# Kernel optimization log

Hardware: AMD Instinct MI355X
Metric: run time of the kernel (lower is better)

Reference implementation:

```python
import jax, jax.numpy as jnp
from jax import lax
import numpy as np

SCALE, K_UP = 2, 5


def conv2d(x, w, pad=0, dil=1):
    return lax.conv_general_dilated(x, w, (1, 1), [(pad, pad), (pad, pad)],
                                    rhs_dilation=(dil, dil),
                                    dimension_numbers=('NCHW', 'OIHW', 'NCHW'))


def cbr(x, w, g, b, pad=0, relu=True):
    # Conv (no bias) + BatchNorm (eval: running_mean=0, running_var=1, eps=1e-5) + optional ReLU
    x = conv2d(x, w, pad)
    x = x * (g / jnp.sqrt(1.0 + 1e-5))[None, :, None, None] + b[None, :, None, None]
    return jnp.maximum(x, 0.0) if relu else x


def resize_bilinear_ac(x, ho, wo):
    # bilinear interpolation, align_corners=True (matches F.interpolate)
    B, C, H, W = x.shape
    ys = jnp.linspace(0.0, H - 1.0, ho)
    xs = jnp.linspace(0.0, W - 1.0, wo)
    y0 = jnp.floor(ys).astype(jnp.int32); y1 = jnp.minimum(y0 + 1, H - 1)
    x0 = jnp.floor(xs).astype(jnp.int32); x1 = jnp.minimum(x0 + 1, W - 1)
    wy = (ys - y0).astype(x.dtype)
    wx = (xs - x0).astype(x.dtype)
    top = x[:, :, y0, :]
    bot = x[:, :, y1, :]
    v = top * (1.0 - wy)[None, None, :, None] + bot * wy[None, None, :, None]
    return v[:, :, :, x0] * (1.0 - wx) + v[:, :, :, x1] * wx


def setup_inputs() -> dict:
    key = jax.random.key(0)
    ks = jax.random.split(key, 10)
    B, CH, CL, H, W = 4, 256, 128, 64, 64
    CMID, CO, IC, KENC = 64, 128, 64, 3

    def wgt(k, shape):
        fan = int(np.prod(shape[1:]))
        return (jax.random.normal(k, shape, jnp.float32) / np.sqrt(fan)).astype(jnp.float32)

    d = {}
    d['x_h'] = jax.random.normal(ks[0], (B, CH, H, W), jnp.float32)
    d['x_l'] = jax.random.normal(ks[1], (B, CL, H * SCALE, W * SCALE), jnp.float32)
    d['w_reduce'] = wgt(ks[2], (IC, CH, 3, 3)); d['g_reduce'] = jnp.ones(IC); d['b_reduce'] = jnp.zeros(IC)
    d['w1'] = wgt(ks[3], (CMID, CH, 1, 1)); d['g1'] = jnp.ones(CMID); d['b1'] = jnp.zeros(CMID)
    d['w2'] = wgt(ks[4], (CMID, CL, 1, 1)); d['g2'] = jnp.ones(CMID); d['b2'] = jnp.zeros(CMID)
    d['w_enc'] = wgt(ks[5], (K_UP * K_UP, 2 * CMID, KENC, KENC)); d['g_enc'] = jnp.ones(K_UP * K_UP); d['b_enc'] = jnp.zeros(K_UP * K_UP)
    d['w_out1'] = wgt(ks[6], (CO, IC + CL, 3, 3)); d['g_out1'] = jnp.ones(CO); d['b_out1'] = jnp.zeros(CO)
    d['w_out2'] = wgt(ks[7], (CO, CO, 1, 1)); d['g_out2'] = jnp.ones(CO); d['b_out2'] = jnp.zeros(CO)
    return d


def reference(x_h, x_l, w_reduce, g_reduce, b_reduce, w1, g1, b1, w2, g2, b2,
              w_enc, g_enc, b_enc, w_out1, g_out1, b_out1, w_out2, g_out2, b_out2):
    b, c, h, w = x_h.shape
    h_, w_ = h * SCALE, w * SCALE
    # content encoder -> per-pixel reassembly kernels
    x1 = resize_bilinear_ac(cbr(x_h, w1, g1, b1), h_, w_)          # [b, cmid, h_, w_]
    x2 = cbr(x_l, w2, g2, b2)                                       # [b, cmid, h_, w_]
    Wm = cbr(jnp.concatenate([x1, x2], axis=1), w_enc, g_enc, b_enc, pad=1, relu=False)
    Wm = jax.nn.softmax(Wm, axis=1)                                  # [b, k_up^2, h_, w_]
    # reduced high-level features, upsampled
    xr = cbr(x_h, w_reduce, g_reduce, b_reduce, pad=1)               # [b, ic, h, w]
    xu = resize_bilinear_ac(xr, h_, w_)                              # [b, ic, h_, w_]
    # CARAFE-style reassembly: unfold(k=5, dilation=2, pad=4) expressed as
    # 25 shifted windows of the zero-padded map -> no k^2-blown buffer.
    pad = (K_UP // 2) * SCALE
    xp = jnp.pad(xu, ((0, 0), (0, 0), (pad, pad), (pad, pad)))
    X = jnp.zeros_like(xu)
    for i in range(K_UP):
        for j in range(K_UP):
            win = xp[:, :, i * SCALE:i * SCALE + h_, j * SCALE:j * SCALE + w_]
            X = X + Wm[:, i * K_UP + j][:, None] * win
    y = jnp.concatenate([X, x_l], axis=1)
    y = cbr(y, w_out1, g_out1, b_out1, pad=1)
    y = cbr(y, w_out2, g_out2, b_out2)
    return y
```

## Files before the change

kernel.cpp:

```cpp
#include <hip/hip_runtime.h>
#include <math.h>

#define BNS 0.99999500003749981f

typedef short          bf16x8  __attribute__((ext_vector_type(8)));
typedef float          f32x4   __attribute__((ext_vector_type(4)));
typedef unsigned short u16x8   __attribute__((ext_vector_type(8)));
typedef unsigned short u16x4   __attribute__((ext_vector_type(4)));
typedef unsigned short ushort_t;

__device__ inline ushort_t f2b(float f) {
    union { float f; unsigned int u; } x; x.f = f;
    unsigned int u = x.u;
    unsigned int r = (u + 0x7FFFu + ((u >> 16) & 1u)) >> 16;
    return (ushort_t)r;
}
__device__ inline float b2f(ushort_t s) {
    union { unsigned int u; float f; } x; x.u = ((unsigned int)s) << 16;
    return x.f;
}

__device__ inline void glds16(const ushort_t* gp, void* lp) {
    __builtin_amdgcn_global_load_lds(
        (const __attribute__((address_space(1))) unsigned int*)gp,
        (__attribute__((address_space(3))) unsigned int*)lp, 16, 0, 0);
}

template<int N, bool LG0>
__device__ __forceinline__ void wait_v() {
    if constexpr (LG0) {
        if constexpr (N == 0)  asm volatile("s_waitcnt vmcnt(0) lgkmcnt(0)" ::: "memory");
        if constexpr (N == 2)  asm volatile("s_waitcnt vmcnt(2) lgkmcnt(0)" ::: "memory");
        if constexpr (N == 3)  asm volatile("s_waitcnt vmcnt(3) lgkmcnt(0)" ::: "memory");
        if constexpr (N == 4)  asm volatile("s_waitcnt vmcnt(4) lgkmcnt(0)" ::: "memory");
        if constexpr (N == 5)  asm volatile("s_waitcnt vmcnt(5) lgkmcnt(0)" ::: "memory");
        if constexpr (N == 6)  asm volatile("s_waitcnt vmcnt(6) lgkmcnt(0)" ::: "memory");
        if constexpr (N == 8)  asm volatile("s_waitcnt vmcnt(8) lgkmcnt(0)" ::: "memory");
        if constexpr (N == 9)  asm volatile("s_waitcnt vmcnt(9) lgkmcnt(0)" ::: "memory");
        if constexpr (N == 10) asm volatile("s_waitcnt vmcnt(10) lgkmcnt(0)" ::: "memory");
        if constexpr (N == 12) asm volatile("s_waitcnt vmcnt(12) lgkmcnt(0)" ::: "memory");
        if constexpr (N == 16) asm volatile("s_waitcnt vmcnt(16) lgkmcnt(0)" ::: "memory");
    } else {
        if constexpr (N == 0)  asm volatile("s_waitcnt vmcnt(0)" ::: "memory");
        if constexpr (N == 2)  asm volatile("s_waitcnt vmcnt(2)" ::: "memory");
        if constexpr (N == 3)  asm volatile("s_waitcnt vmcnt(3)" ::: "memory");
        if constexpr (N == 4)  asm volatile("s_waitcnt vmcnt(4)" ::: "memory");
        if constexpr (N == 5)  asm volatile("s_waitcnt vmcnt(5)" ::: "memory");
        if constexpr (N == 6)  asm volatile("s_waitcnt vmcnt(6)" ::: "memory");
        if constexpr (N == 8)  asm volatile("s_waitcnt vmcnt(8)" ::: "memory");
        if constexpr (N == 9)  asm volatile("s_waitcnt vmcnt(9)" ::: "memory");
        if constexpr (N == 10) asm volatile("s_waitcnt vmcnt(10)" ::: "memory");
        if constexpr (N == 12) asm volatile("s_waitcnt vmcnt(12)" ::: "memory");
        if constexpr (N == 16) asm volatile("s_waitcnt vmcnt(16)" ::: "memory");
    }
}
#define WAITSW(nn, LG) do { switch (nn) {                       \
    case 0:  wait_v<0,  LG>(); break;                           \
    case 2:  wait_v<2,  LG>(); break;                           \
    case 3:  wait_v<3,  LG>(); break;                           \
    case 4:  wait_v<4,  LG>(); break;                           \
    case 5:  wait_v<5,  LG>(); break;                           \
    case 6:  wait_v<6,  LG>(); break;                           \
    case 8:  wait_v<8,  LG>(); break;                           \
    case 9:  wait_v<9,  LG>(); break;                           \
    case 10: wait_v<10, LG>(); break;                           \
    case 12: wait_v<12, LG>(); break;                           \
    default: wait_v<16, LG>(); break; } } while (0)

#define E_BWR   0u
#define E_BW1   147456u
#define E_BW2   163840u
#define E_BWE   172032u
#define E_BWO1  208896u
#define E_BWO2  430080u
#define E_ZP    446464u
#define OFF_R1  524288u
#define OFF_R4  4718592u
#define OFF_R2  8912896u
#define OFF_R3  9961472u
#define OFF_R6  11010048u
#define OFF_R5  13107200u


__device__ inline void wseg3(int idx, const float* src, ushort_t* dst,
                             int TAPS, int COT, int CIT, int CO_real) {
    int kt  = idx / (COT * 32);
    int r   = idx - kt * (COT * 32);
    int q   = r / (COT * 8);
    int r2  = r - q * (COT * 8);
    int co  = r2 >> 3;
    int e   = r2 & 7;
    int KCT = CIT >> 5;
    int tap = kt / KCT, j = kt - tap * KCT;
    int ci  = j * 32 + q * 8 + e;
    float v = (co < CO_real) ? src[((size_t)co * CIT + ci) * TAPS + tap] : 0.f;
    dst[idx] = f2b(v);
}

__device__ inline void cvt_t16(const float* __restrict__ in,
                               ushort_t* __restrict__ out,
                               int C, int LHW, int px, int npx) {
    if (px >= npx) return;
    int HW = 1 << LHW;
    int b = px >> LHW, phw = px & (HW - 1);
    const float* src = in + (size_t)b * C * HW + phw;
    unsigned base = (unsigned)(px >> 4) * (C * 16) + (unsigned)(px & 15) * 8;
    for (int c0 = 0; c0 < C; c0 += 8) {
        u16x8 o;
#pragma unroll
        for (int j = 0; j < 8; j++) o[j] = f2b(src[(size_t)(c0 + j) * HW]);
        *reinterpret_cast<u16x8*>(out + base + (c0 >> 3) * 128) = o;
    }
}

__global__ __launch_bounds__(256)
void prep_all(const float* wr, const float* w1, const float* w2,
              const float* we, const float* wo1, const float* wo2,
              const float* xh, const float* xl, ushort_t* ws0)
{
    int bx = blockIdx.x;
    int tid = threadIdx.x;
    if (bx < 1872) {
        int idx = bx * 256 + tid;
        const int n0 = 9*64*256;
        const int n1 = 64*256;
        const int n2 = 64*128;
        const int n3 = 9*32*128;
        const int n4 = 9*128*192;
        const int n5 = 128*128;
        if (idx < n0) { wseg3(idx, wr,  ws0 + E_BWR,  9, 64, 256, 64);  return; } idx -= n0;
        if (idx < n1) { wseg3(idx, w1,  ws0 + E_BW1,  1, 64, 256, 64);  return; } idx -= n1;
        if (idx < n2) { wseg3(idx, w2,  ws0 + E_BW2,  1, 64, 128, 64);  return; } idx -= n2;
        if (idx < n3) { wseg3(idx, we,  ws0 + E_BWE,  9, 32, 128, 25);  return; } idx -= n3;
        if (idx < n4) { wseg3(idx, wo1, ws0 + E_BWO1, 9, 128, 192, 128); return; } idx -= n4;
        if (idx < n5) { wseg3(idx, wo2, ws0 + E_BWO2, 1, 128, 128, 128); return; } idx -= n5;
        if (idx < 32768) ws0[E_ZP + idx] = 0;
        return;
    }
    bx -= 1872;
    if (bx < 64) { cvt_t16(xh, ws0 + OFF_R1, 256, 12, bx * 256 + tid, 16384); return; }
    bx -= 64;
    cvt_t16(xl, ws0 + OFF_R5, 128, 14, bx * 256 + tid, 65536);
}

__global__ __launch_bounds__(256)
void conv_dual(const ushort_t* __restrict__ ws0,
               unsigned offA, unsigned offWr, unsigned offW1,
               const float* __restrict__ gR, const float* __restrict__ bR,
               const float* __restrict__ g1, const float* __restrict__ b1,
               ushort_t* __restrict__ outR, ushort_t* __restrict__ outC)
{
    constexpr int BM = 64, BN = 64, KCT = 8, DEP = 3, NPH = 24;
    constexpr int MF = 2, NF = 2;
    constexpr int WOFF = BM * 64;
    constexpr int ZS   = WOFF + 4 * BN * 64;
    constexpr int BUF  = ZS + 16;
    __shared__ __align__(16) char lds[DEP * BUF];

    const unsigned nx = gridDim.x, ox = blockIdx.x;
    const unsigned qq = nx >> 3, xcd = ox & 7, k0 = ox >> 3;
    const unsigned bx = xcd * qq + k0;

    const int tid = threadIdx.x, w = tid >> 6, lane = tid & 63;
    const int l15 = lane & 15, lhi = lane >> 4;
    const int wpx = (w & 1) * 32, cw0 = (w >> 1) * 32;
    const int yb = (int)(bx & 63u);
    const unsigned pxc0 = bx * 4;

    if (tid < 4 * DEP) *(unsigned*)(lds + (tid >> 2) * BUF + ZS + (tid & 3) * 4) = 0u;

    int aA[3][MF];
#pragma unroll
    for (int dxi = 0; dxi < 3; ++dxi)
#pragma unroll
        for (int mf = 0; mf < MF; ++mf) {
            int pr = wpx + mf * 16 + l15 + dxi - 1;
            bool ok = (pr >= 0) && (pr < BM);
            aA[dxi][mf] = ok ? (((pr >> 4) << 10) + (lhi << 8) + ((pr & 15) << 4)) : ZS;
        }
    int wA[NF];
#pragma unroll
    for (int nf = 0; nf < NF; ++nf)
        wA[nf] = lhi * 1024 + (cw0 + nf * 16 + l15) * 16;

    f32x4 acc[NF][MF], acc2[NF][MF];
#pragma unroll
    for (int nf = 0; nf < NF; ++nf)
#pragma unroll
        for (int mf = 0; mf < MF; ++mf) {
            acc[nf][mf]  = (f32x4){0.f, 0.f, 0.f, 0.f};
            acc2[nf][mf] = (f32x4){0.f, 0.f, 0.f, 0.f};
        }

    auto stage = [&](int p, int bsel) {
        char* lb = lds + bsel * BUF;
        const int dyi = p >> 3, kc = p & 7;
        const int dy = dyi - 1;
        const bool rowv = (yb + dy >= 0) && (yb + dy < 64);
        unsigned s = rowv
            ? offA + (unsigned)((int)pxc0 + dy * 4 + w) * 4096u
                   + (unsigned)(kc * 512) + (unsigned)(lane * 8)
            : E_ZP + (unsigned)(lane * 8);
        glds16(ws0 + s, lb + w * 1024);
#pragma unroll
        for (int i = 0; i < 3; ++i) {
            int t3 = i * 4 + w;
            int tl = t3 >> 2, uu = t3 & 3;
            unsigned wsrc = offWr + (unsigned)(((dyi * 3 + tl) * KCT + kc) * 2048)
                          + (unsigned)(uu * 512) + (unsigned)(lane * 8);
            glds16(ws0 + wsrc, lb + WOFF + tl * 4096 + uu * 1024);
        }
        if (dyi == 1) {
            unsigned wsrc = offW1 + (unsigned)(kc * 2048)
                          + (unsigned)(w * 512) + (unsigned)(lane * 8);
            glds16(ws0 + wsrc, lb + WOFF + 3 * 4096 + w * 1024);
        }
    };

    auto step = [&](int p, int bsel) {
        const char* lb = lds + bsel * BUF;
        const int dyi = p >> 3;
        __builtin_amdgcn_s_setprio(1);
#pragma unroll
        for (int t = 0; t < 3; ++t) {
            bf16x8 af[MF], wf[NF];
#pragma unroll
            for (int mf = 0; mf < MF; ++mf)
                af[mf] = *reinterpret_cast<const bf16x8*>(lb + aA[t][mf]);
#pragma unroll
            for (int nf = 0; nf < NF; ++nf)
                wf[nf] = *reinterpret_cast<const bf16x8*>(lb + WOFF + t * 4096 + wA[nf]);
#pragma unroll
            for (int nf = 0; nf < NF; ++nf)
#pragma unroll
                for (int mf = 0; mf < MF; ++mf)
                    acc[nf][mf] = __builtin_amdgcn_mfma_f32_16x16x32_bf16(
                        wf[nf], af[mf], acc[nf][mf], 0, 0, 0);
        }
        if (dyi == 1) {
            bf16x8 af[MF], wf[NF];
#pragma unroll
            for (int mf = 0; mf < MF; ++mf)
                af[mf] = *reinterpret_cast<const bf16x8*>(lb + aA[1][mf]);
#pragma unroll
            for (int nf = 0; nf < NF; ++nf)
                wf[nf] = *reinterpret_cast<const bf16x8*>(lb + WOFF + 3 * 4096 + wA[nf]);
#pragma unroll
            for (int nf = 0; nf < NF; ++nf)
#pragma unroll
                for (int mf = 0; mf < MF; ++mf)
                    acc2[nf][mf] = __builtin_amdgcn_mfma_f32_16x16x32_bf16(
                        wf[nf], af[mf], acc2[nf][mf], 0, 0, 0);
        }
        __builtin_amdgcn_s_setprio(0);
    };

    stage(0, 0); stage(1, 1);
#pragma unroll
    for (int p = 0; p < NPH; ++p) {
        if (p + 2 < NPH) stage(p + 2, (p + 2) % 3);
        int n1 = (p + 1 < NPH) ? ((((p + 1) >> 3) == 1) ? 5 : 4) : 0;
        int n2 = (p + 2 < NPH) ? ((((p + 2) >> 3) == 1) ? 5 : 4) : 0;
        int nn = n1 + n2;
        if (p == 0) WAITSW(nn, true); else WAITSW(nn, false);
        __builtin_amdgcn_s_barrier();
        __builtin_amdgcn_sched_barrier(0);
        step(p, p % 3);
        __builtin_amdgcn_sched_barrier(0);
        if (p + 1 < NPH) __builtin_amdgcn_s_barrier();
    }

#pragma unroll
    for (int which = 0; which < 2; ++which) {
        const float* gg = which ? g1 : gR;
        const float* bb = which ? b1 : bR;
        ushort_t* oo = which ? outC : outR;
#pragma unroll
        for (int nf = 0; nf < NF; ++nf) {
            const int cg = cw0 + nf * 16 + (lhi << 2);
            float sc[4], bi[4];
#pragma unroll
            for (int r = 0; r < 4; r++) { sc[r] = gg[cg + r] * BNS; bi[r] = bb[cg + r]; }
#pragma unroll
            for (int mf = 0; mf < MF; ++mf) {
                f32x4 a = which ? acc2[nf][mf] : acc[nf][mf];
                u16x4 ov;
#pragma unroll
                for (int r = 0; r < 4; r++)
                    ov[r] = f2b(fmaxf(fmaf(a[r], sc[r], bi[r]), 0.f));
                int px = (int)bx * BM + wpx + mf * 16 + l15;
                unsigned off = (unsigned)(px >> 4) * 1024
                             + (unsigned)(cg >> 3) * 128
                             + (unsigned)(px & 15) * 8 + (unsigned)(cg & 7);
                *reinterpret_cast<u16x4*>(oo + off) = ov;
            }
        }
    }
}

template<int TAPS, int BM, int CIA, int CIB, int COT, int BN, int G,
         int WSX, int DEP, int EPI>
__global__ __launch_bounds__(256)
void conv_lds(const ushort_t* __restrict__ ws0,
              unsigned offA, unsigned offB, unsigned offW,
              const float* __restrict__ g, const float* __restrict__ bia,
              int COclamp, void* __restrict__ outp,
              int H, int LHW, int relu)
{
    constexpr int KCA = CIA / 32, KCB = CIB / 32;
    constexpr int KCT = KCA + KCB;
    constexpr int NW  = (TAPS == 9) ? 3 : G;
    constexpr int ACP = (TAPS == 9) ? 1 : G;
    constexpr int NPH = (TAPS == 9) ? 3 * KCT : KCT / G;
    constexpr int WSY = 4 / WSX;
    constexpr int MF = BM / WSX / 16;
    constexpr int NF = BN / WSY / 16;
    constexpr int ACHUNK = BM / 16;
    constexpr int A4 = (ACP * ACHUNK + 3) / 4;
    constexpr int WUNIT = BN / 16;
    constexpr int TWU = NW * WUNIT;
    constexpr int W4 = (TWU + 3) / 4;
    constexpr int SS = A4 + W4;
    constexpr int WOFF = ACP * BM * 64;
    constexpr int ZS   = WOFF + NW * BN * 64;
    constexpr int BUF  = ZS + 16;
    constexpr int LBN3 = (BN == 128) ? 10 : (BN == 64) ? 9 : 8;
    __shared__ __align__(16) char lds[DEP * BUF];

    const unsigned nx = gridDim.x, ox = blockIdx.x;
    const unsigned qq = nx >> 3, xcd = ox & 7, k0 = ox >> 3;
    const unsigned bx = xcd * qq + k0;
    const int co_blk = blockIdx.y * BN;

    const int tid = threadIdx.x, w = tid >> 6, lane = tid & 63;
    const int l15 = lane & 15, lhi = lane >> 4;
    const int wpx = (w % WSX) * (BM / WSX);
    const int cw0 = (w / WSX) * (BN / WSY);
    const int yb = (int)(bx & (unsigned)(H - 1));
    const unsigned pxc0 = bx * ACHUNK;

    if (tid < 4 * DEP) *(unsigned*)(lds + (tid >> 2) * BUF + ZS + (tid & 3) * 4) = 0u;

    int aA[3][MF];
#pragma unroll
    for (int dxi = 0; dxi < 3; ++dxi) {
        const int dx = dxi - 1;
#pragma unroll
        for (int mf = 0; mf < MF; ++mf) {
            int pr = wpx + mf * 16 + l15 + dx;
            bool ok = (TAPS == 1) ? true : (pr >= 0 && pr < BM);
            aA[dxi][mf] = ok ? (((pr >> 4) << 10) + (lhi << 8) + ((pr & 15) << 4)) : ZS;
        }
    }
    int wA[NF];
#pragma unroll
    for (int nf = 0; nf < NF; ++nf)
        wA[nf] = (lhi * BN + cw0 + nf * 16 + l15) * 16;

    f32x4 acc[NF][MF];
#pragma unroll
    for (int nf = 0; nf < NF; ++nf)
#pragma unroll
        for (int mf = 0; mf < MF; ++mf)
            acc[nf][mf] = (f32x4){0.f, 0.f, 0.f, 0.f};

    auto stage = [&](int p, int bsel) {
        char* lb = lds + bsel * BUF;
        if constexpr (TAPS == 9) {
            const int dyi = p / KCT, kc = p - dyi * KCT;
            const int dy = dyi - 1;
            const bool isA = (kc < KCA);
            const int kcs = isA ? kc : kc - KCA;
            const int CI  = isA ? CIA : CIB;
            const unsigned offS = isA ? offA : offB;
            const bool rowv = (yb + dy >= 0) && (yb + dy < H);
#pragma unroll
            for (int i = 0; i < A4; ++i) {
                int u = (i * 4 + w) % ACHUNK;
                unsigned s = rowv
                    ? offS + (unsigned)((int)pxc0 + dy * ACHUNK + u) * (unsigned)(CI * 16)
                           + (unsigned)(kcs * 512) + (unsigned)(lane * 8)
                    : E_ZP + (unsigned)(lane * 8);
                glds16(ws0 + s, lb + u * 1024);
            }
#pragma unroll
            for (int i = 0; i < W4; ++i) {
                int t3 = (i * 4 + w) % TWU;
                int tl = t3 / WUNIT, uu = t3 - tl * WUNIT;
                unsigned wsrc = offW + (unsigned)((dyi * 3 + tl) * KCT + kc)
                                       * (unsigned)(COT * 32);
                int el  = uu * 512 + lane * 8;
                int q   = el >> LBN3;
                int col = (el & ((1 << LBN3) - 1)) >> 3;
                glds16(ws0 + wsrc + q * (COT * 8) + (co_blk + col) * 8,
                       lb + WOFF + tl * (BN * 64) + uu * 1024);
            }
        } else {
#pragma unroll
            for (int i = 0; i < A4; ++i) {
                int lin = (i * 4 + w) % (ACP * ACHUNK);
                int gc = lin / ACHUNK, u = lin - gc * ACHUNK;
                unsigned s = offA + (unsigned)(pxc0 + u) * (unsigned)(CIA * 16)
                           + (unsigned)((p * G + gc) * 512) + (unsigned)(lane * 8);
                glds16(ws0 + s, lb + gc * (BM * 64) + u * 1024);
            }
#pragma unroll
            for (int i = 0; i < W4; ++i) {
                int t3 = (i * 4 + w) % TWU;
                int tl = t3 / WUNIT, uu = t3 - tl * WUNIT;
                unsigned wsrc = offW + (unsigned)(p * G + tl) * (unsigned)(COT * 32);
                int el  = uu * 512 + lane * 8;
                int q   = el >> LBN3;
                int col = (el & ((1 << LBN3) - 1)) >> 3;
                glds16(ws0 + wsrc + q * (COT * 8) + (co_blk + col) * 8,
                       lb + WOFF + tl * (BN * 64) + uu * 1024);
            }
        }
    };

    auto step = [&](int p, int bsel) {
        const char* lb = lds + bsel * BUF;
        __builtin_amdgcn_s_setprio(1);
#pragma unroll
        for (int t = 0; t < NW; ++t) {
            const int dxi = (TAPS == 9) ? t : 1;
            const char* ab = lb + ((TAPS == 9) ? 0 : t * (BM * 64));
            bf16x8 af[MF], wf[NF];
#pragma unroll
            for (int mf = 0; mf < MF; ++mf)
                af[mf] = *reinterpret_cast<const bf16x8*>(ab + aA[dxi][mf]);
#pragma unroll
            for (int nf = 0; nf < NF; ++nf)
                wf[nf] = *reinterpret_cast<const bf16x8*>(
                    lb + WOFF + t * (BN * 64) + wA[nf]);
#pragma unroll
            for (int nf = 0; nf < NF; ++nf)
#pragma unroll
                for (int mf = 0; mf < MF; ++mf)
                    acc[nf][mf] = __builtin_amdgcn_mfma_f32_16x16x32_bf16(
                        wf[nf], af[mf], acc[nf][mf], 0, 0, 0);
        }
        __builtin_amdgcn_s_setprio(0);
    };

    stage(0, 0);
    if constexpr (DEP == 3) { if (1 < NPH) stage(1, 1); }
#pragma unroll
    for (int p = 0; p < NPH; ++p) {
        if (p + DEP - 1 < NPH) stage(p + DEP - 1, (p + DEP - 1) % DEP);
        int rem = NPH - 1 - p;
        int nn = (rem >= DEP - 1 ? DEP - 1 : rem) * SS;
        if (p == 0) WAITSW(nn, true); else WAITSW(nn, false);
        __builtin_amdgcn_s_barrier();
        __builtin_amdgcn_sched_barrier(0);
        step(p, p % DEP);
        __builtin_amdgcn_sched_barrier(0);
        if (p + 1 < NPH) __builtin_amdgcn_s_barrier();
    }

    if constexpr (EPI == 0) {
        ushort_t* o1 = (ushort_t*)outp;
#pragma unroll
        for (int nf = 0; nf < NF; ++nf) {
            const int cg = co_blk + cw0 + nf * 16 + (lhi << 2);
            float sc[4], bi[4];
#pragma unroll
            for (int r = 0; r < 4; r++) {
                int c = min(cg + r, COclamp - 1);
                sc[r] = g[c] * BNS; bi[r] = bia[c];
            }
#pragma unroll
            for (int mf = 0; mf < MF; ++mf) {
                f32x4 a = acc[nf][mf];
                u16x4 ov;
#pragma unroll
                for (int r = 0; r < 4; r++) {
                    float v = fmaf(a[r], sc[r], bi[r]);
                    if (relu) v = fmaxf(v, 0.f);
                    ov[r] = f2b(v);
                }
                int px = (int)bx * BM + wpx + mf * 16 + l15;
                unsigned off = (unsigned)(px >> 4) * (COT * 16)
                             + (unsigned)(cg >> 3) * 128
                             + (unsigned)(px & 15) * 8 + (unsigned)(cg & 7);
                *reinterpret_cast<u16x4*>(o1 + off) = ov;
            }
        }
    } else if constexpr (EPI == 1) {
        float* o1 = (float*)outp;
        const int HW = 1 << LHW;
#pragma unroll
        for (int nf = 0; nf < NF; ++nf) {
            const int cg = co_blk + cw0 + nf * 16 + (lhi << 2);
            float sc[4], bi[4];
#pragma unroll
            for (int r = 0; r < 4; r++) {
                int c = min(cg + r, COclamp - 1);
                sc[r] = g[c] * BNS; bi[r] = bia[c];
            }
#pragma unroll
            for (int mf = 0; mf < MF; ++mf) {
                int px = (int)bx * BM + wpx + mf * 16 + l15;
                int b = px >> LHW, phw = px & (HW - 1);
#pragma unroll
                for (int r = 0; r < 4; r++) {
                    float v = fmaf(acc[nf][mf][r], sc[r], bi[r]);
                    if (relu) v = fmaxf(v, 0.f);
                    o1[((size_t)(b * COT + cg + r)) * HW + phw] = v;
                }
            }
        }
    } else if constexpr (EPI == 2) {
        __syncthreads();
        float* sf = (float*)lds;
#pragma unroll
        for (int nf = 0; nf < NF; ++nf) {
            const int cg = cw0 + nf * 16 + (lhi << 2);
#pragma unroll
            for (int mf = 0; mf < MF; ++mf) {
                int pxl = wpx + mf * 16 + l15;
                f32x4 a = acc[nf][mf];
#pragma unroll
                for (int r = 0; r < 4; r++) {
                    int c = min(cg + r, COclamp - 1);
                    sf[(cg + r) * 136 + pxl] = fmaf(a[r], g[c] * BNS, bia[c]);
                }
            }
        }
        __syncthreads();
        if (tid < BM) {
            int gpx = (int)bx * BM + tid;
            float v[25];
#pragma unroll
            for (int c = 0; c < 25; ++c) v[c] = sf[c * 136 + tid];
            float m = v[0];
#pragma unroll
            for (int c = 1; c < 25; ++c) m = fmaxf(m, v[c]);
            float s = 0.f;
#pragma unroll
            for (int c = 0; c < 25; ++c) { v[c] = __expf(v[c] - m); s += v[c]; }
            float inv = 1.f / s;
            ushort_t* o1 = (ushort_t*)outp;
            unsigned base = (unsigned)(gpx >> 4) * (32 * 16) + (unsigned)(gpx & 15) * 8;
#pragma unroll
            for (int q = 0; q < 3; ++q) {
                u16x8 ov;
#pragma unroll
                for (int k = 0; k < 8; k++) ov[k] = f2b(v[q * 8 + k] * inv);
                *reinterpret_cast<u16x8*>(o1 + base + q * 128) = ov;
            }
            o1[base + 384] = f2b(v[24] * inv);
        }
    } else {
        float* o1 = (float*)outp;
        float* sf = (float*)lds;
        const int phw_base = (int)((bx & 127u) * 128);
        const int bimg = (int)(bx >> 7);
        const int lane32 = tid & 31, cog = tid >> 5;
#pragma unroll
        for (int c = 0; c < 2; ++c) {
            __syncthreads();
            if (cw0 == c * 64) {
#pragma unroll
                for (int nf = 0; nf < NF; ++nf) {
                    const int cgl = nf * 16 + (lhi << 2);
                    const int cg  = c * 64 + cgl;
                    float sc[4], bi[4];
#pragma unroll
                    for (int r = 0; r < 4; r++) { sc[r] = g[cg + r] * BNS; bi[r] = bia[cg + r]; }
#pragma unroll
                    for (int mf = 0; mf < MF; ++mf) {
                        int pxl = wpx + mf * 16 + l15;
                        f32x4 a = acc[nf][mf];
#pragma unroll
                        for (int r = 0; r < 4; r++) {
                            float v = fmaf(a[r], sc[r], bi[r]);
                            if (relu) v = fmaxf(v, 0.f);
                            sf[(cgl + r) * 132 + pxl] = v;
                        }
                    }
                }
            }
            __syncthreads();
#pragma unroll
            for (int j = 0; j < 8; ++j) {
                int col = cog + j * 8;
                f32x4 v = *reinterpret_cast<const f32x4*>(sf + col * 132 + lane32 * 4);
                *reinterpret_cast<f32x4*>(
                    o1 + (((size_t)bimg * 128 + c * 64 + col) << 14)
                       + phw_base + lane32 * 4) = v;
            }
        }
    }
}

__global__ __launch_bounds__(256)
void resize2x_t16(const ushort_t* __restrict__ in, ushort_t* __restrict__ out)
{
    int t = blockIdx.x * 256 + threadIdx.x;
    int cg = t & 7;
    int opx = t >> 3;
    int xo = opx & 127;
    int rest = opx >> 7;
    int yo = rest & 127;
    int b  = rest >> 7;
    float fy = (float)yo * 63.f / 127.f;
    float fx = (float)xo * 63.f / 127.f;
    int y0 = (int)fy, x0 = (int)fx;
    float wy = fy - (float)y0, wx = fx - (float)x0;
    int y1 = min(y0 + 1, 63), x1 = min(x0 + 1, 63);
    int qb = b * 4096;
#define RD(Y, X) (*reinterpret_cast<const bf16x8*>(in + \
    (unsigned)(((qb + (Y) * 64 + (X)) >> 4) * 1024) + cg * 128 + ((qb + (Y) * 64 + (X)) & 15) * 8))
    bf16x8 v00 = RD(y0, x0), v01 = RD(y0, x1), v10 = RD(y1, x0), v11 = RD(y1, x1);
#undef RD
    u16x8 o;
#pragma unroll
    for (int k = 0; k < 8; k++) {
        float l = b2f((ushort_t)v00[k]) * (1.f - wy) + b2f((ushort_t)v10[k]) * wy;
        float r = b2f((ushort_t)v01[k]) * (1.f - wy) + b2f((ushort_t)v11[k]) * wy;
        o[k] = f2b(l * (1.f - wx) + r * wx);
    }
    *reinterpret_cast<u16x8*>(out + (unsigned)(opx >> 4) * 1024 + cg * 128 + (opx & 15) * 8) = o;
}

__global__ __launch_bounds__(256)
void carafe25(const ushort_t* __restrict__ wm, const ushort_t* __restrict__ xu,
              ushort_t* __restrict__ out)
{
    int t = blockIdx.x * 256 + threadIdx.x;
    int cg = t & 7;
    int px = t >> 3;
    int x = px & 127;
    int y = (px >> 7) & 127;
    const ushort_t* wp = wm + (unsigned)(px >> 4) * 512 + (px & 15) * 8;
    u16x8 r0 = *reinterpret_cast<const u16x8*>(wp);
    u16x8 r1 = *reinterpret_cast<const u16x8*>(wp + 128);
    u16x8 r2 = *reinterpret_cast<const u16x8*>(wp + 256);
    float v[25];
#pragma unroll
    for (int k = 0; k < 8; k++) v[k]      = b2f(r0[k]);
#pragma unroll
    for (int k = 0; k < 8; k++) v[8 + k]  = b2f(r1[k]);
#pragma unroll
    for (int k = 0; k < 8; k++) v[16 + k] = b2f(r2[k]);
    v[24] = b2f(wp[384]);

    float acc[8];
#pragma unroll
    for (int k = 0; k < 8; k++) acc[k] = 0.f;
#pragma unroll
    for (int i = 0; i < 5; i++) {
        int yy = y + 2 * i - 4;
#pragma unroll
        for (int j = 0; j < 5; j++) {
            int xx = x + 2 * j - 4;
            if (yy >= 0 && yy < 128 && xx >= 0 && xx < 128) {
                int q = px + (2 * i - 4) * 128 + (2 * j - 4);
                bf16x8 xv = *reinterpret_cast<const bf16x8*>(
                    xu + (unsigned)(q >> 4) * 1024 + cg * 128 + (q & 15) * 8);
                float wv = v[i * 5 + j];
#pragma unroll
                for (int k = 0; k < 8; k++)
                    acc[k] = fmaf(wv, b2f((ushort_t)xv[k]), acc[k]);
            }
        }
    }
    u16x8 o;
#pragma unroll
    for (int k = 0; k < 8; k++) o[k] = f2b(acc[k]);
    *reinterpret_cast<u16x8*>(out + (unsigned)(px >> 4) * 1024 + cg * 128 + (px & 15) * 8) = o;
}

extern "C" void kernel_launch(void* const* d_in, const int* in_sizes, int n_in,
                              void* d_out, int out_size, void* d_ws, size_t ws_size,
                              hipStream_t stream)
{
    const float* x_h      = (const float*)d_in[0];
    const float* x_l      = (const float*)d_in[1];
    const float* w_reduce = (const float*)d_in[2];
    const float* g_reduce = (const float*)d_in[3];
    const float* b_reduce = (const float*)d_in[4];
    const float* w1       = (const float*)d_in[5];
    const float* g1       = (const float*)d_in[6];
    const float* b1       = (const float*)d_in[7];
    const float* w2       = (const float*)d_in[8];
    const float* g2       = (const float*)d_in[9];
    const float* b2       = (const float*)d_in[10];
    const float* w_enc    = (const float*)d_in[11];
    const float* g_enc    = (const float*)d_in[12];
    const float* b_enc    = (const float*)d_in[13];
    const float* w_out1   = (const float*)d_in[14];
    const float* g_out1   = (const float*)d_in[15];
    const float* b_out1   = (const float*)d_in[16];
    const float* w_out2   = (const float*)d_in[17];
    const float* g_out2   = (const float*)d_in[18];
    const float* b_out2   = (const float*)d_in[19];

    ushort_t* ws0 = (ushort_t*)d_ws;

    const unsigned oXHC = OFF_R1;
    const unsigned oC1  = OFF_R2;
    const unsigned oXR  = OFF_R3;
    const unsigned oX1  = OFF_R4;
    const unsigned oXLC = OFF_R5;
    const unsigned oX2  = OFF_R1;
    const unsigned oWM  = OFF_R6;
    const unsigned oXU  = OFF_R4;
    const unsigned oXB  = OFF_R1;
    const unsigned oY1  = OFF_R4;

    prep_all<<<2192, 256, 0, stream>>>(w_reduce, w1, w2, w_enc, w_out1, w_out2,
                                       x_h, x_l, ws0);
    conv_dual<<<256, 256, 0, stream>>>(
        ws0, oXHC, E_BWR, E_BW1, g_reduce, b_reduce, g1, b1,
        ws0 + oXR, ws0 + oC1);
    resize2x_t16<<<2048, 256, 0, stream>>>(ws0 + oC1, ws0 + oX1);
    conv_lds<1, 128, 128, 0, 64, 64, 1, 2, 3, 0><<<dim3(512, 1), 256, 0, stream>>>(
        ws0, oXLC, 0u, E_BW2, g2, b2, 64, ws0 + oX2, 128, 14, 1);
    conv_lds<9, 128, 64, 64, 32, 32, 1, 4, 3, 2><<<dim3(512, 1), 256, 0, stream>>>(
        ws0, oX1, oX2, E_BWE, g_enc, b_enc, 25, ws0 + oWM, 128, 14, 0);
    resize2x_t16<<<2048, 256, 0, stream>>>(ws0 + oXR, ws0 + oXU);
    carafe25<<<2048, 256, 0, stream>>>(ws0 + oWM, ws0 + oXU, ws0 + oXB);
    conv_lds<9, 128, 64, 128, 128, 128, 1, 2, 2, 0><<<dim3(512, 1), 256, 0, stream>>>(
        ws0, oXB, oXLC, E_BWO1, g_out1, b_out1, 128, ws0 + oY1, 128, 14, 1);
    conv_lds<1, 128, 128, 0, 128, 128, 2, 2, 2, 3><<<dim3(512, 1), 256, 0, stream>>>(
        ws0, oY1, 0u, E_BWO2, g_out2, b_out2, 128, d_out, 128, 14, 1);
}
```

Baseline: 133.9 us.

## Fuse final 1x1 conv into the 3x3 output conv epilogue

The last 3x3 conv+BN+ReLU now keeps its 128-pixel by 128-channel bf16 result tile in LDS. The same block loads the 1x1 weights and runs a second MFMA GEMM over it, then writes the fp32 output directly. This drops one kernel launch and the global round-trip of the intermediate Y1 tensor. In exchange the block does more work serially in its epilogue and uses more LDS and registers (a second accumulator array), which may lower occupancy.

```diff
diff --git a/kernel.cpp b/kernel.cpp
--- a/kernel.cpp
+++ b/kernel.cpp
@@ -305,7 +305,9 @@
               unsigned offA, unsigned offB, unsigned offW,
               const float* __restrict__ g, const float* __restrict__ bia,
               int COclamp, void* __restrict__ outp,
-              int H, int LHW, int relu)
+              int H, int LHW, int relu,
+              unsigned offW2, const float* __restrict__ g2,
+              const float* __restrict__ bia2)
 {
     constexpr int KCA = CIA / 32, KCB = CIB / 32;
     constexpr int KCT = KCA + KCB;
@@ -552,6 +554,67 @@
             o1[base + 384] = f2b(v[24] * inv);
         }
     } else {
+#pragma unroll
+        for (int nf = 0; nf < NF; ++nf) {
+            const int cg = cw0 + nf * 16 + (lhi << 2);
+            float sc[4], bi[4];
+#pragma unroll
+            for (int r = 0; r < 4; r++) { sc[r] = g[cg + r] * BNS; bi[r] = bia[cg + r]; }
+#pragma unroll
+            for (int mf = 0; mf < MF; ++mf) {
+                f32x4 a = acc[nf][mf];
+                u16x4 ov;
+#pragma unroll
+                for (int r = 0; r < 4; r++)
+                    ov[r] = f2b(fmaxf(fmaf(a[r], sc[r], bi[r]), 0.f));
+                int pxl = wpx + mf * 16 + l15;
+                unsigned off = (unsigned)(pxl >> 4) * 4096
+                             + (unsigned)(cg >> 5) * 1024
+                             + (unsigned)((cg >> 3) & 3) * 256
+                             + (unsigned)(pxl & 15) * 16 + (unsigned)(cg & 7) * 2;
+                *reinterpret_cast<u16x4*>((char*)lds + off) = ov;
+            }
+        }
+        __syncthreads();
+#pragma unroll
+        for (int i = 0; i < 8; ++i) {
+            int U = i * 4 + w;
+            glds16(ws0 + offW2 + (unsigned)U * 512 + (unsigned)(lane * 8),
+                   lds + BUF + U * 1024);
+        }
+        wait_v<0, true>();
+        __builtin_amdgcn_s_barrier();
+        __builtin_amdgcn_sched_barrier(0);
+        f32x4 acc2[NF][MF];
+#pragma unroll
+        for (int nf = 0; nf < NF; ++nf)
+#pragma unroll
+            for (int mf = 0; mf < MF; ++mf)
+                acc2[nf][mf] = (f32x4){0.f, 0.f, 0.f, 0.f};
+        __builtin_amdgcn_s_setprio(1);
+#pragma unroll
+        for (int kc = 0; kc < 4; ++kc) {
+            bf16x8 af[MF], wf[NF];
+#pragma unroll
+            for (int mf = 0; mf < MF; ++mf) {
+                int pxl = wpx + mf * 16 + l15;
+                af[mf] = *reinterpret_cast<const bf16x8*>(
+                    (char*)lds + (pxl >> 4) * 4096 + kc * 1024
+                               + (lhi << 8) + (pxl & 15) * 16);
+            }
+#pragma unroll
+            for (int nf = 0; nf < NF; ++nf)
+                wf[nf] = *reinterpret_cast<const bf16x8*>(
+                    (char*)lds + BUF + kc * 8192 + wA[nf]);
+#pragma unroll
+            for (int nf = 0; nf < NF; ++nf)
+#pragma unroll
+                for (int mf = 0; mf < MF; ++mf)
+                    acc2[nf][mf] = __builtin_amdgcn_mfma_f32_16x16x32_bf16(
+                        wf[nf], af[mf], acc2[nf][mf], 0, 0, 0);
+        }
+        __builtin_amdgcn_s_setprio(0);
+        __syncthreads();
         float* o1 = (float*)outp;
         float* sf = (float*)lds;
         const int phw_base = (int)((bx & 127u) * 128);
@@ -559,7 +622,7 @@
         const int lane32 = tid & 31, cog = tid >> 5;
 #pragma unroll
         for (int c = 0; c < 2; ++c) {
-            __syncthreads();
+            if (c) __syncthreads();
             if (cw0 == c * 64) {
 #pragma unroll
                 for (int nf = 0; nf < NF; ++nf) {
@@ -567,17 +630,15 @@
                     const int cg  = c * 64 + cgl;
                     float sc[4], bi[4];
 #pragma unroll
-                    for (int r = 0; r < 4; r++) { sc[r] = g[cg + r] * BNS; bi[r] = bia[cg + r]; }
+                    for (int r = 0; r < 4; r++) { sc[r] = g2[cg + r] * BNS; bi[r] = bia2[cg + r]; }
 #pragma unroll
                     for (int mf = 0; mf < MF; ++mf) {
                         int pxl = wpx + mf * 16 + l15;
-                        f32x4 a = acc[nf][mf];
-#pragma unroll
-                        for (int r = 0; r < 4; r++) {
-                            float v = fmaf(a[r], sc[r], bi[r]);
-                            if (relu) v = fmaxf(v, 0.f);
-                            sf[(cgl + r) * 132 + pxl] = v;
-                        }
+                        f32x4 a = acc2[nf][mf];
+#pragma unroll
+                        for (int r = 0; r < 4; r++)
+                            sf[(cgl + r) * 132 + pxl] =
+                                fmaxf(fmaf(a[r], sc[r], bi[r]), 0.f);
                     }
                 }
             }
@@ -708,7 +769,6 @@
     const unsigned oWM  = OFF_R6;
     const unsigned oXU  = OFF_R4;
     const unsigned oXB  = OFF_R1;
-    const unsigned oY1  = OFF_R4;
 
     prep_all<<<2192, 256, 0, stream>>>(w_reduce, w1, w2, w_enc, w_out1, w_out2,
                                        x_h, x_l, ws0);
@@ -717,13 +777,14 @@
         ws0 + oXR, ws0 + oC1);
     resize2x_t16<<<2048, 256, 0, stream>>>(ws0 + oC1, ws0 + oX1);
     conv_lds<1, 128, 128, 0, 64, 64, 1, 2, 3, 0><<<dim3(512, 1), 256, 0, stream>>>(
-        ws0, oXLC, 0u, E_BW2, g2, b2, 64, ws0 + oX2, 128, 14, 1);
+        ws0, oXLC, 0u, E_BW2, g2, b2, 64, ws0 + oX2, 128, 14, 1,
+        0u, nullptr, nullptr);
     conv_lds<9, 128, 64, 64, 32, 32, 1, 4, 3, 2><<<dim3(512, 1), 256, 0, stream>>>(
-        ws0, oX1, oX2, E_BWE, g_enc, b_enc, 25, ws0 + oWM, 128, 14, 0);
+        ws0, oX1, oX2, E_BWE, g_enc, b_enc, 25, ws0 + oWM, 128, 14, 0,
+        0u, nullptr, nullptr);
     resize2x_t16<<<2048, 256, 0, stream>>>(ws0 + oXR, ws0 + oXU);
     carafe25<<<2048, 256, 0, stream>>>(ws0 + oWM, ws0 + oXU, ws0 + oXB);
-    conv_lds<9, 128, 64, 128, 128, 128, 1, 2, 2, 0><<<dim3(512, 1), 256, 0, stream>>>(
-        ws0, oXB, oXLC, E_BWO1, g_out1, b_out1, 128, ws0 + oY1, 128, 14, 1);
-    conv_lds<1, 128, 128, 0, 128, 128, 2, 2, 2, 3><<<dim3(512, 1), 256, 0, stream>>>(
-        ws0, oY1, 0u, E_BWO2, g_out2, b_out2, 128, d_out, 128, 14, 1);
-}
+    conv_lds<9, 128, 64, 128, 128, 128, 1, 2, 2, 4><<<dim3(512, 1), 256, 0, stream>>>(
+        ws0, oXB, oXLC, E_BWO1, g_out1, b_out1, 128, d_out, 128, 14, 1,
+        E_BWO2, g_out2, b_out2);
+}
```

Measured after the change: 128.7 us. -3.9%, faster.
